# Performance work log

Measured on AMD Instinct MI355X. Metric: run time of the kernel, lower is better.

Reference implementation:

```python
import jax, jax.numpy as jnp
import numpy as np

V, E, H = 50257, 256, 128          # vocab, embedding_size, lstm hidden per direction
L, B = 2048, 64                    # seq_len, batch (x is [L, B], seq-first)
SEP, MASK = 50256, 0
SEP_EVERY = 16
N_UTT = L // SEP_EVERY             # utterances per sequence (seps planted regularly)


def setup_inputs() -> dict:
    key = jax.random.key(0)
    ks = jax.random.split(key, 12)
    x = jax.random.randint(ks[0], (L, B), 0, SEP, dtype=jnp.int32)
    # plant sep tokens every SEP_EVERY positions -> each utterance has SEP_EVERY tokens
    x = x.at[SEP_EVERY - 1::SEP_EVERY, :].set(SEP)
    s = 1.0 / np.sqrt(H)
    u = lambda k, sh: jax.random.uniform(k, sh, jnp.float32, -s, s)
    return {
        "x": x,
        "emb": jax.random.normal(ks[1], (V, E), jnp.float32),
        "w_ih_f": u(ks[2], (4 * H, E)), "w_hh_f": u(ks[3], (4 * H, H)),
        "b_ih_f": u(ks[4], (4 * H,)),   "b_hh_f": u(ks[5], (4 * H,)),
        "w_ih_b": u(ks[6], (4 * H, E)), "w_hh_b": u(ks[7], (4 * H, H)),
        "b_ih_b": u(ks[8], (4 * H,)),   "b_hh_b": u(ks[9], (4 * H,)),
        "w_out": u(ks[10], (2, E)),     "b_out": u(ks[11], (2,)),
    }


def _lstm_dir(xu, w_ih, w_hh, b_ih, b_hh, reverse):
    # xu: [T, B, E]; PyTorch LSTM gate order i, f, g, o
    xp = jnp.einsum("tbe,ge->tbg", xu, w_ih) + b_ih + b_hh  # [T, B, 4H]

    def step(carry, xt):
        h, c = carry
        g = xt + h @ w_hh.T
        i, f, gg, o = jnp.split(g, 4, axis=-1)
        c = jax.nn.sigmoid(f) * c + jax.nn.sigmoid(i) * jnp.tanh(gg)
        h = jax.nn.sigmoid(o) * jnp.tanh(c)
        return (h, c), h

    init = (jnp.zeros((xu.shape[1], H), xu.dtype), jnp.zeros((xu.shape[1], H), xu.dtype))
    _, hs = jax.lax.scan(step, init, xp, reverse=reverse)
    return hs  # [T, B, H]


def _forward(x, emb, w_ih_f, w_hh_f, b_ih_f, b_hh_f, w_ih_b, w_hh_b, b_ih_b, b_hh_b, w_out, b_out):
    # --- ragged utterance mean-pool (replaces per-token Python loops) ---
    seps = (x == SEP)
    seg = jnp.cumsum(seps.astype(jnp.int32), axis=0) - seps.astype(jnp.int32)  # [L,B]: utterance id per token (sep ends its utterance)
    gids = (seg * B + jnp.arange(B, dtype=jnp.int32)[None, :]).reshape(L * B)
    tok_emb = emb[x]                                              # [L, B, E]
    sums = jax.ops.segment_sum(tok_emb.reshape(L * B, E), gids, num_segments=N_UTT * B).reshape(N_UTT, B, E)
    cnts = jax.ops.segment_sum(jnp.ones((L * B,), tok_emb.dtype), gids, num_segments=N_UTT * B).reshape(N_UTT, B, 1)
    u = jnp.where(cnts > 0, sums / jnp.maximum(cnts, 1.0), 0.0)   # [N_UTT, B, E] (zeros pad, as original)
    # --- BiLSTM over utterances ---
    h_f = _lstm_dir(u, w_ih_f, w_hh_f, b_ih_f, b_hh_f, reverse=False)
    h_b = _lstm_dir(u, w_ih_b, w_hh_b, b_ih_b, b_hh_b, reverse=True)
    h = jnp.concatenate([h_f, h_b], axis=-1)                      # [N_UTT, B, E]
    logits = jnp.einsum("tbe,oe->tbo", h, w_out) + b_out          # [N_UTT, B, 2]
    policy = jax.nn.softmax(logits, axis=-1)
    # greedy policy (deterministic reference)
    u_mask = jnp.argmax(policy, axis=-1)                          # [N_UTT, B] in {0,1}
    chosen_policy = jnp.take_along_axis(policy, u_mask[..., None], axis=-1)  # [N_UTT, B, 1]
    # expand utterance mask to token mask and mask the input
    token_mask = u_mask.astype(bool)[seg, jnp.arange(B)[None, :]]  # [L, B]
    masked_input = jnp.where(token_mask, x, MASK)
    return logits, policy, chosen_policy, u_mask.astype(bool), masked_input


def reference(x, emb, w_ih_f, w_hh_f, b_ih_f, b_hh_f, w_ih_b, w_hh_b, b_ih_b, b_hh_b, w_out, b_out):
    return _forward(x, emb, w_ih_f, w_hh_f, b_ih_f, b_hh_f, w_ih_b, w_hh_b, b_ih_b, b_hh_b, w_out, b_out)
```

## Files before the change

kernel.cpp:

```cpp
#include <hip/hip_runtime.h>
#include <hip/hip_fp16.h>
#include <math.h>

#define LL   2048
#define BB   64
#define EE   256
#define HH   128
#define GG   512
#define TT   128
#define SEPT 50256

__global__ __launch_bounds__(256) void segscan_k(
    const int* __restrict__ x, int* __restrict__ seg,
    int* __restrict__ cnt, int* __restrict__ start)
{
    int b   = blockIdx.x;
    int tid = threadIdx.x;
    __shared__ int tsum[256];
    __shared__ int ucnt[TT];
    __shared__ int ustart[TT];

    int flags[8];
    int local = 0;
#pragma unroll
    for (int i = 0; i < 8; i++) {
        int t = tid * 8 + i;
        flags[i] = (x[t * BB + b] == SEPT) ? 1 : 0;
        local += flags[i];
    }
    tsum[tid] = local;
    __syncthreads();
    int val = local;
    for (int off = 1; off < 256; off <<= 1) {
        int other = (tid >= off) ? tsum[tid - off] : 0;
        __syncthreads();
        val += other;
        tsum[tid] = val;
        __syncthreads();
    }
    int excl = val - local;

    if (tid < TT) ucnt[tid] = 0;
    __syncthreads();
    int run = excl;
#pragma unroll
    for (int i = 0; i < 8; i++) {
        int t = tid * 8 + i;
        int s = run;
        seg[t * BB + b] = s;
        run += flags[i];
        if (s < TT) atomicAdd(&ucnt[s], 1);
    }
    __syncthreads();
    if (tid == 0) {
        int acc = 0;
        for (int u = 0; u < TT; u++) { ustart[u] = acc; acc += ucnt[u]; }
    }
    __syncthreads();
    if (tid < TT) {
        cnt[tid * BB + b]   = ucnt[tid];
        start[tid * BB + b] = ustart[tid];
    }
}

__global__ __launch_bounds__(256) void pool_k(
    const int* __restrict__ x, const float* __restrict__ emb,
    const int* __restrict__ cnt, const int* __restrict__ start,
    float* __restrict__ up)
{
    int wid  = threadIdx.x >> 6;
    int lane = threadIdx.x & 63;
    int bid  = blockIdx.x * 4 + wid;
    int b    = bid & 63;
    int c    = cnt[bid];
    int st   = start[bid];

    float4 acc = {0.f, 0.f, 0.f, 0.f};
    int tok = (c > 0) ? x[st * BB + b] : 0;
    for (int j = 0; j < c; j++) {
        int tok_n = (j + 1 < c) ? x[(st + j + 1) * BB + b] : 0;
        float4 v = ((const float4*)(emb + (size_t)tok * EE))[lane];
        acc.x += v.x; acc.y += v.y; acc.z += v.z; acc.w += v.w;
        tok = tok_n;
    }
    float inv = (c > 0) ? 1.f / (float)c : 0.f;
    float4 r = {acc.x * inv, acc.y * inv, acc.z * inv, acc.w * inv};
    ((float4*)(up + (size_t)bid * EE))[lane] = r;
}

__global__ __launch_bounds__(256) void xp_gemm_k(
    const float* __restrict__ A,
    const float* __restrict__ wf, const float* __restrict__ wb,
    const float* __restrict__ bihf, const float* __restrict__ bhhf,
    const float* __restrict__ bihb, const float* __restrict__ bhhb,
    float* __restrict__ C)
{
    __shared__ float As[32][128];
    __shared__ float Bs[32][128];
    int tid  = threadIdx.x;
    int row0 = blockIdx.x * 128;
    int col0 = blockIdx.y * 128;
    int tx = tid & 15, ty = tid >> 4;
    float acc[8][8] = {};

    for (int k0 = 0; k0 < EE; k0 += 32) {
#pragma unroll
        for (int i = 0; i < 4; i++) {
            int idx = tid + i * 256;
            int m   = idx >> 3;
            int k4  = idx & 7;
            float4 av = *(const float4*)(A + (size_t)(row0 + m) * EE + k0 + k4 * 4);
            As[k4 * 4 + 0][m] = av.x; As[k4 * 4 + 1][m] = av.y;
            As[k4 * 4 + 2][m] = av.z; As[k4 * 4 + 3][m] = av.w;
        }
#pragma unroll
        for (int i = 0; i < 4; i++) {
            int idx = tid + i * 256;
            int n   = idx >> 3;
            int k4  = idx & 7;
            int gc  = col0 + n;
            const float* wsrc = (gc < GG) ? (wf + (size_t)gc * EE)
                                          : (wb + (size_t)(gc - GG) * EE);
            float4 bv = *(const float4*)(wsrc + k0 + k4 * 4);
            Bs[k4 * 4 + 0][n] = bv.x; Bs[k4 * 4 + 1][n] = bv.y;
            Bs[k4 * 4 + 2][n] = bv.z; Bs[k4 * 4 + 3][n] = bv.w;
        }
        __syncthreads();
#pragma unroll
        for (int k = 0; k < 32; k++) {
            float a8[8], b8[8];
            *(float4*)&a8[0] = *(const float4*)&As[k][ty * 8 + 0];
            *(float4*)&a8[4] = *(const float4*)&As[k][ty * 8 + 4];
            *(float4*)&b8[0] = *(const float4*)&Bs[k][tx * 8 + 0];
            *(float4*)&b8[4] = *(const float4*)&Bs[k][tx * 8 + 4];
#pragma unroll
            for (int i = 0; i < 8; i++)
#pragma unroll
                for (int j = 0; j < 8; j++)
                    acc[i][j] += a8[i] * b8[j];
        }
        __syncthreads();
    }

    float bias[8];
#pragma unroll
    for (int j = 0; j < 8; j++) {
        int gc = col0 + tx * 8 + j;
        bias[j] = (gc < GG) ? (bihf[gc] + bhhf[gc])
                            : (bihb[gc - GG] + bhhb[gc - GG]);
    }
#pragma unroll
    for (int i = 0; i < 8; i++) {
        int r = row0 + ty * 8 + i;
        float4 v0 = {acc[i][0] + bias[0], acc[i][1] + bias[1],
                     acc[i][2] + bias[2], acc[i][3] + bias[3]};
        float4 v1 = {acc[i][4] + bias[4], acc[i][5] + bias[5],
                     acc[i][6] + bias[6], acc[i][7] + bias[7]};
        *(float4*)(C + (size_t)r * 1024 + col0 + tx * 8 + 0) = v0;
        *(float4*)(C + (size_t)r * 1024 + col0 + tx * 8 + 4) = v1;
    }
}

__device__ __forceinline__ float sigm_f(float x) {
    return 1.f / (1.f + __expf(-x));
}
__device__ __forceinline__ float tanh_f(float x) {
    return 1.f - 2.f / (__expf(2.f * x) + 1.f);
}

__global__ __launch_bounds__(256) void cvt_k(
    const float* __restrict__ wf, const float* __restrict__ wb,
    __half* __restrict__ o)
{
    int i = blockIdx.x * 256 + threadIdx.x;
    int k   = i & 15;
    int l   = (i >> 4) & 63;
    int j   = (i >> 10) & 7;
    int wv  = (i >> 13) & 7;
    int dir = i >> 16;
    const float* src = dir ? wb : wf;
    o[i] = __float2half(src[(l + 64 * j) * HH + 16 * wv + k]);
}

__global__ __launch_bounds__(512, 2) void lstm_rec_k(
    const float* __restrict__ xp,
    const __half* __restrict__ wh16,
    float* __restrict__ hout)
{
    int bid = blockIdx.x;
    int dir = bid >> 6;
    int b   = bid & 63;
    int tid = threadIdx.x;
    int wv  = tid >> 6;
    int l   = tid & 63;
    const __half* wh = wh16 + (size_t)dir * (GG * HH);
    const __half* wbase = wh + (((size_t)wv * 8) * 64 + l) * 16;

    __shared__ __align__(16) float h_lds[HH];
    __shared__ float part[GG][9];
    __shared__ float act[GG];

    int g    = tid;
    int sect = g >> 7;

    float c = 0.f;
    if (g < HH) h_lds[g] = 0.f;
    __syncthreads();

    int t0   = dir ? (TT - 1) : 0;
    float xg = xp[(size_t)(t0 * BB + b) * 1024 + dir * GG + g];

    for (int s = 0; s < TT; s++) {
        float hs[16];
#pragma unroll
        for (int k4 = 0; k4 < 4; k4++)
            *(float4*)&hs[k4 * 4] = *(const float4*)&h_lds[wv * 16 + k4 * 4];

        float acc[8] = {0.f, 0.f, 0.f, 0.f, 0.f, 0.f, 0.f, 0.f};
#pragma unroll
        for (int j = 0; j < 8; j++) {
            float4 q0 = *(const float4*)(wbase + (size_t)j * 1024);
            float4 q1 = *(const float4*)(wbase + (size_t)j * 1024 + 8);
            const __half2* ha = (const __half2*)&q0;
            const __half2* hb = (const __half2*)&q1;
#pragma unroll
            for (int p = 0; p < 4; p++) {
                acc[j] = fmaf(__low2float(ha[p]),  hs[2 * p + 0], acc[j]);
                acc[j] = fmaf(__high2float(ha[p]), hs[2 * p + 1], acc[j]);
            }
#pragma unroll
            for (int p = 0; p < 4; p++) {
                acc[j] = fmaf(__low2float(hb[p]),  hs[8 + 2 * p + 0], acc[j]);
                acc[j] = fmaf(__high2float(hb[p]), hs[8 + 2 * p + 1], acc[j]);
            }
        }

        float xg_next = xg;
        if (s < TT - 1) {
            int tn = dir ? (TT - 2 - s) : (s + 1);
            xg_next = xp[(size_t)(tn * BB + b) * 1024 + dir * GG + g];
        }

#pragma unroll
        for (int j = 0; j < 8; j++)
            part[l + 64 * j][wv] = acc[j];
        __syncthreads();

        float sum = xg;
#pragma unroll
        for (int w2 = 0; w2 < 8; w2++)
            sum += part[g][w2];
        act[g] = (sect == 2) ? tanh_f(sum) : sigm_f(sum);
        __syncthreads();

        if (tid < HH) {
            float si = act[tid], sf = act[HH + tid];
            float tg = act[2 * HH + tid], so = act[3 * HH + tid];
            c = sf * c + si * tg;
            float h = so * tanh_f(c);
            h_lds[tid] = h;
            int t = dir ? (TT - 1 - s) : s;
            hout[((size_t)(dir * TT + t) * BB + b) * HH + tid] = h;
        }
        xg = xg_next;
        __syncthreads();
    }
}

__global__ __launch_bounds__(256) void head_k(
    const float* __restrict__ hbuf,
    const float* __restrict__ wout, const float* __restrict__ bout,
    float* __restrict__ out)
{
    int wid  = threadIdx.x >> 6;
    int lane = threadIdx.x & 63;
    int row  = blockIdx.x * 4 + wid;
    int t = row >> 6, b = row & 63;
    const float* hf = hbuf + ((size_t)(t)      * BB + b) * HH;
    const float* hb = hbuf + ((size_t)(TT + t) * BB + b) * HH;

    float l0 = 0.f, l1 = 0.f, v;
    v = hf[lane];      l0 += v * wout[lane];           l1 += v * wout[256 + lane];
    v = hf[lane + 64]; l0 += v * wout[64 + lane];      l1 += v * wout[320 + lane];
    v = hb[lane];      l0 += v * wout[128 + lane];     l1 += v * wout[384 + lane];
    v = hb[lane + 64]; l0 += v * wout[192 + lane];     l1 += v * wout[448 + lane];
#pragma unroll
    for (int off = 32; off > 0; off >>= 1) {
        l0 += __shfl_down(l0, off);
        l1 += __shfl_down(l1, off);
    }
    if (lane == 0) {
        l0 += bout[0]; l1 += bout[1];
        float m  = fmaxf(l0, l1);
        float e0 = __expf(l0 - m), e1 = __expf(l1 - m);
        float inv = 1.f / (e0 + e1);
        float p0 = e0 * inv, p1 = e1 * inv;
        int amax = (l1 > l0) ? 1 : 0;
        out[(size_t)row * 2 + 0] = l0;
        out[(size_t)row * 2 + 1] = l1;
        out[16384 + (size_t)row * 2 + 0] = p0;
        out[16384 + (size_t)row * 2 + 1] = p1;
        out[32768 + row] = amax ? p1 : p0;
        out[40960 + row] = (float)amax;
    }
}

__global__ __launch_bounds__(256) void mask_k(
    const int* __restrict__ x, const int* __restrict__ seg,
    const float* __restrict__ umask, float* __restrict__ out4)
{
    int idx = blockIdx.x * 256 + threadIdx.x;
    int b = idx & 63;
    int s = seg[idx];
    if (s > TT - 1) s = TT - 1;
    if (s < 0) s = 0;
    float keep = umask[s * BB + b];
    out4[idx] = (keep != 0.f) ? (float)x[idx] : 0.f;
}

extern "C" void kernel_launch(void* const* d_in, const int* in_sizes, int n_in,
                              void* d_out, int out_size, void* d_ws, size_t ws_size,
                              hipStream_t stream)
{
    const int*   x    = (const int*)  d_in[0];
    const float* emb  = (const float*)d_in[1];
    const float* wihf = (const float*)d_in[2];
    const float* whhf = (const float*)d_in[3];
    const float* bihf = (const float*)d_in[4];
    const float* bhhf = (const float*)d_in[5];
    const float* wihb = (const float*)d_in[6];
    const float* whhb = (const float*)d_in[7];
    const float* bihb = (const float*)d_in[8];
    const float* bhhb = (const float*)d_in[9];
    const float* wout = (const float*)d_in[10];
    const float* bout = (const float*)d_in[11];
    float* out = (float*)d_out;
    char*  ws  = (char*)d_ws;

    int*   seg   = (int*)  (ws + 0);
    int*   cnt   = (int*)  (ws + 524288);
    int*   start = (int*)  (ws + 557056);
    float* up    = (float*)(ws + 589824);
    float* xp    = (float*)(ws + 8978432);
    float* hbuf  = (float*)(ws + 42532864);
    __half* wh16 = (__half*)up;

    segscan_k<<<64, 256, 0, stream>>>(x, seg, cnt, start);
    pool_k<<<2048, 256, 0, stream>>>(x, emb, cnt, start, up);
    xp_gemm_k<<<dim3(64, 8), 256, 0, stream>>>(up, wihf, wihb, bihf, bhhf, bihb, bhhb, xp);
    cvt_k<<<512, 256, 0, stream>>>(whhf, whhb, wh16);
    lstm_rec_k<<<128, 512, 0, stream>>>(xp, wh16, hbuf);
    head_k<<<2048, 256, 0, stream>>>(hbuf, wout, bout, out);
    mask_k<<<512, 256, 0, stream>>>(x, seg, out + 40960, out + 49152);
}
```

Measured before the change: 294.8 us.

## Use fp16 dot2 for recurrent matvec and cache part of W_hh in LDS

The recurrent step now keeps h in fp16 in shared memory and does the W_hh·h product with packed fp16 fdot2 instructions instead of converting each half to float and using scalar FMAs. About 3/8 of each direction's weight slice (48 KB) is staged once into LDS, and the rest is still read from global/L2 every step. The goal is fewer ALU instructions per step and less global weight traffic on the serial critical path. In exchange, h is rounded to fp16, which reduces precision, and the larger LDS footprint may lower occupancy under the 2-block launch bound.

```diff
diff --git a/kernel.cpp b/kernel.cpp
--- a/kernel.cpp
+++ b/kernel.cpp
@@ -182,6 +182,12 @@
     o[i] = __float2half(src[(l + 64 * j) * HH + 16 * wv + k]);
 }
 
+typedef _Float16 h2v __attribute__((ext_vector_type(2)));
+__device__ __forceinline__ float dot2h(unsigned wbits, unsigned hbits, float c) {
+    return __builtin_amdgcn_fdot2(__builtin_bit_cast(h2v, wbits),
+                                  __builtin_bit_cast(h2v, hbits), c, false);
+}
+
 __global__ __launch_bounds__(512, 2) void lstm_rec_k(
     const float* __restrict__ xp,
     const __half* __restrict__ wh16,
@@ -196,43 +202,71 @@
     const __half* wh = wh16 + (size_t)dir * (GG * HH);
     const __half* wbase = wh + (((size_t)wv * 8) * 64 + l) * 16;
 
-    __shared__ __align__(16) float h_lds[HH];
+    __shared__ __align__(16) __half ldsW[24576];
+    __shared__ __align__(16) __half h16_lds[HH];
     __shared__ float part[GG][9];
     __shared__ float act[GG];
 
+#pragma unroll
+    for (int t = 0; t < 6; t++) {
+        int cc  = tid + t * 512;
+        int l2  = cc & 63;
+        int hf  = (cc >> 6) & 1;
+        int rem = cc >> 7;
+        int jj  = rem % 3;
+        int wv2 = rem / 3;
+        const __half* src = wh + (((size_t)(wv2 * 8 + jj) * 64 + l2) * 16 + hf * 8);
+        *(uint4*)(ldsW + (size_t)cc * 8) = *(const uint4*)src;
+    }
+
     int g    = tid;
     int sect = g >> 7;
 
     float c = 0.f;
-    if (g < HH) h_lds[g] = 0.f;
-    __syncthreads();
+    if (tid < HH) h16_lds[tid] = __float2half(0.f);
+    __syncthreads();
+
+    const uint4* ldsW4 = (const uint4*)ldsW;
+    const uint4* h16v  = (const uint4*)h16_lds;
 
     int t0   = dir ? (TT - 1) : 0;
     float xg = xp[(size_t)(t0 * BB + b) * 1024 + dir * GG + g];
 
     for (int s = 0; s < TT; s++) {
-        float hs[16];
-#pragma unroll
-        for (int k4 = 0; k4 < 4; k4++)
-            *(float4*)&hs[k4 * 4] = *(const float4*)&h_lds[wv * 16 + k4 * 4];
+        unsigned hhv[8];
+        {
+            uint4 ha  = h16v[wv * 2 + 0];
+            uint4 hbq = h16v[wv * 2 + 1];
+            hhv[0] = ha.x;  hhv[1] = ha.y;  hhv[2] = ha.z;  hhv[3] = ha.w;
+            hhv[4] = hbq.x; hhv[5] = hbq.y; hhv[6] = hbq.z; hhv[7] = hbq.w;
+        }
 
         float acc[8] = {0.f, 0.f, 0.f, 0.f, 0.f, 0.f, 0.f, 0.f};
 #pragma unroll
-        for (int j = 0; j < 8; j++) {
-            float4 q0 = *(const float4*)(wbase + (size_t)j * 1024);
-            float4 q1 = *(const float4*)(wbase + (size_t)j * 1024 + 8);
-            const __half2* ha = (const __half2*)&q0;
-            const __half2* hb = (const __half2*)&q1;
-#pragma unroll
-            for (int p = 0; p < 4; p++) {
-                acc[j] = fmaf(__low2float(ha[p]),  hs[2 * p + 0], acc[j]);
-                acc[j] = fmaf(__high2float(ha[p]), hs[2 * p + 1], acc[j]);
-            }
-#pragma unroll
-            for (int p = 0; p < 4; p++) {
-                acc[j] = fmaf(__low2float(hb[p]),  hs[8 + 2 * p + 0], acc[j]);
-                acc[j] = fmaf(__high2float(hb[p]), hs[8 + 2 * p + 1], acc[j]);
-            }
+        for (int jj = 0; jj < 3; jj++) {
+            uint4 w0 = ldsW4[((wv * 3 + jj) * 2 + 0) * 64 + l];
+            uint4 w1 = ldsW4[((wv * 3 + jj) * 2 + 1) * 64 + l];
+            acc[jj] = dot2h(w0.x, hhv[0], acc[jj]);
+            acc[jj] = dot2h(w0.y, hhv[1], acc[jj]);
+            acc[jj] = dot2h(w0.z, hhv[2], acc[jj]);
+            acc[jj] = dot2h(w0.w, hhv[3], acc[jj]);
+            acc[jj] = dot2h(w1.x, hhv[4], acc[jj]);
+            acc[jj] = dot2h(w1.y, hhv[5], acc[jj]);
+            acc[jj] = dot2h(w1.z, hhv[6], acc[jj]);
+            acc[jj] = dot2h(w1.w, hhv[7], acc[jj]);
+        }
+#pragma unroll
+        for (int j = 3; j < 8; j++) {
+            uint4 q0 = *(const uint4*)(wbase + (size_t)j * 1024);
+            uint4 q1 = *(const uint4*)(wbase + (size_t)j * 1024 + 8);
+            acc[j] = dot2h(q0.x, hhv[0], acc[j]);
+            acc[j] = dot2h(q0.y, hhv[1], acc[j]);
+            acc[j] = dot2h(q0.z, hhv[2], acc[j]);
+            acc[j] = dot2h(q0.w, hhv[3], acc[j]);
+            acc[j] = dot2h(q1.x, hhv[4], acc[j]);
+            acc[j] = dot2h(q1.y, hhv[5], acc[j]);
+            acc[j] = dot2h(q1.z, hhv[6], acc[j]);
+            acc[j] = dot2h(q1.w, hhv[7], acc[j]);
         }
 
         float xg_next = xg;
@@ -258,7 +292,7 @@
             float tg = act[2 * HH + tid], so = act[3 * HH + tid];
             c = sf * c + si * tg;
             float h = so * tanh_f(c);
-            h_lds[tid] = h;
+            h16_lds[tid] = __float2half(h);
             int t = dir ? (TT - 1 - s) : s;
             hout[((size_t)(dir * TT + t) * BB + b) * HH + tid] = h;
         }
```

After: 302.5 us. 1.03x slower.

## Restructure LSTM recurrence: per-thread gate rows, LDS-cached weights, fdot2

Applied to the files above, without the earlier changes.

Each thread now computes one full gate row over all 128 hidden inputs instead of splitting the reduction across 8 waves, which removes the partial-sum LDS buffer and one barrier per timestep. Half of the fp16 recurrent weights are staged once into 64KB of LDS and the rest are streamed from global/L2 each step. The hidden state is stored as fp16 and the dot products use packed fdot2 instructions. This lowers hidden-state precision and raises LDS usage, which may cut the occupancy implied by the two-blocks-per-SM launch bound.

```diff
diff --git a/kernel.cpp b/kernel.cpp
--- a/kernel.cpp
+++ b/kernel.cpp
@@ -173,84 +173,85 @@
     __half* __restrict__ o)
 {
     int i = blockIdx.x * 256 + threadIdx.x;
-    int k   = i & 15;
-    int l   = (i >> 4) & 63;
-    int j   = (i >> 10) & 7;
-    int wv  = (i >> 13) & 7;
+    int e   = i & 7;
+    int g   = (i >> 3) & 511;
+    int q   = (i >> 12) & 15;
     int dir = i >> 16;
     const float* src = dir ? wb : wf;
-    o[i] = __float2half(src[(l + 64 * j) * HH + 16 * wv + k]);
+    o[i] = __float2half(src[(size_t)g * HH + q * 8 + e]);
+}
+
+typedef _Float16 h2v __attribute__((ext_vector_type(2)));
+__device__ __forceinline__ float dot2h(unsigned wbits, unsigned hbits, float c) {
+    return __builtin_amdgcn_fdot2(__builtin_bit_cast(h2v, wbits),
+                                  __builtin_bit_cast(h2v, hbits), c, false);
 }
 
 __global__ __launch_bounds__(512, 2) void lstm_rec_k(
     const float* __restrict__ xp,
-    const __half* __restrict__ wh16,
+    const __half* __restrict__ w16,
     float* __restrict__ hout)
 {
     int bid = blockIdx.x;
     int dir = bid >> 6;
     int b   = bid & 63;
     int tid = threadIdx.x;
-    int wv  = tid >> 6;
-    int l   = tid & 63;
-    const __half* wh = wh16 + (size_t)dir * (GG * HH);
-    const __half* wbase = wh + (((size_t)wv * 8) * 64 + l) * 16;
-
-    __shared__ __align__(16) float h_lds[HH];
-    __shared__ float part[GG][9];
+    int g   = tid;
+    int sect = g >> 7;
+    const uint4* wp = (const uint4*)(w16 + (size_t)dir * (16 * GG * 8));
+
+    __shared__ uint4 wlds[8 * GG];
+    __shared__ __align__(16) __half h16_lds[HH];
     __shared__ float act[GG];
 
-    int g    = tid;
-    int sect = g >> 7;
+#pragma unroll
+    for (int t = 0; t < 8; t++) {
+        int idx = tid + t * 512;
+        wlds[idx] = wp[idx];
+    }
 
     float c = 0.f;
-    if (g < HH) h_lds[g] = 0.f;
-    __syncthreads();
+    if (tid < HH) h16_lds[tid] = __float2half(0.f);
+    __syncthreads();
+
+    const uint4* h16v = (const uint4*)h16_lds;
 
     int t0   = dir ? (TT - 1) : 0;
     float xg = xp[(size_t)(t0 * BB + b) * 1024 + dir * GG + g];
 
     for (int s = 0; s < TT; s++) {
-        float hs[16];
-#pragma unroll
-        for (int k4 = 0; k4 < 4; k4++)
-            *(float4*)&hs[k4 * 4] = *(const float4*)&h_lds[wv * 16 + k4 * 4];
-
-        float acc[8] = {0.f, 0.f, 0.f, 0.f, 0.f, 0.f, 0.f, 0.f};
-#pragma unroll
-        for (int j = 0; j < 8; j++) {
-            float4 q0 = *(const float4*)(wbase + (size_t)j * 1024);
-            float4 q1 = *(const float4*)(wbase + (size_t)j * 1024 + 8);
-            const __half2* ha = (const __half2*)&q0;
-            const __half2* hb = (const __half2*)&q1;
-#pragma unroll
-            for (int p = 0; p < 4; p++) {
-                acc[j] = fmaf(__low2float(ha[p]),  hs[2 * p + 0], acc[j]);
-                acc[j] = fmaf(__high2float(ha[p]), hs[2 * p + 1], acc[j]);
-            }
-#pragma unroll
-            for (int p = 0; p < 4; p++) {
-                acc[j] = fmaf(__low2float(hb[p]),  hs[8 + 2 * p + 0], acc[j]);
-                acc[j] = fmaf(__high2float(hb[p]), hs[8 + 2 * p + 1], acc[j]);
-            }
-        }
+        uint4 q8[8];
+#pragma unroll
+        for (int q = 0; q < 8; q++)
+            q8[q] = wp[(q + 8) * GG + g];
+
+        float acc = xg;
+#pragma unroll
+        for (int q = 0; q < 8; q++) {
+            uint4 w = wlds[q * GG + g];
+            uint4 hv = h16v[q];
+            acc = dot2h(w.x, hv.x, acc);
+            acc = dot2h(w.y, hv.y, acc);
+            acc = dot2h(w.z, hv.z, acc);
+            acc = dot2h(w.w, hv.w, acc);
+        }
+#pragma unroll
+        for (int q = 0; q < 8; q++) {
+            uint4 w = q8[q];
+            uint4 hv = h16v[q + 8];
+            acc = dot2h(w.x, hv.x, acc);
+            acc = dot2h(w.y, hv.y, acc);
+            acc = dot2h(w.z, hv.z, acc);
+            acc = dot2h(w.w, hv.w, acc);
+        }
+
+        act[g] = (sect == 2) ? tanh_f(acc) : sigm_f(acc);
 
         float xg_next = xg;
         if (s < TT - 1) {
             int tn = dir ? (TT - 2 - s) : (s + 1);
             xg_next = xp[(size_t)(tn * BB + b) * 1024 + dir * GG + g];
         }
-
-#pragma unroll
-        for (int j = 0; j < 8; j++)
-            part[l + 64 * j][wv] = acc[j];
-        __syncthreads();
-
-        float sum = xg;
-#pragma unroll
-        for (int w2 = 0; w2 < 8; w2++)
-            sum += part[g][w2];
-        act[g] = (sect == 2) ? tanh_f(sum) : sigm_f(sum);
         __syncthreads();
 
         if (tid < HH) {
@@ -258,7 +259,7 @@
             float tg = act[2 * HH + tid], so = act[3 * HH + tid];
             c = sf * c + si * tg;
             float h = so * tanh_f(c);
-            h_lds[tid] = h;
+            h16_lds[tid] = __float2half(h);
             int t = dir ? (TT - 1 - s) : s;
             hout[((size_t)(dir * TT + t) * BB + b) * HH + tid] = h;
         }
```

After: 288.1 us. 1.02x faster.
